# Performance work log

Measured on AMD Instinct MI355X. Metric: run time of the kernel, lower is better.

Reference implementation:

```python
import jax, jax.numpy as jnp
import numpy as np
from jax.ops import segment_sum, segment_max

B, P, NP, EP = 128, 16, 256, 1280
EPG, ODIM, NH = 2048, 256, 128
EPS = 1e-5


def _bn(x, g, b):
    # BatchNorm1d (training-mode batch statistics), biased variance like torch
    mu = x.mean(0)
    var = ((x - mu) ** 2).mean(0)
    return g * (x - mu) * jax.lax.rsqrt(var + EPS) + b


def _gat(feat, src, dst, W, al, ar, resW, bias):
    # DGL GATConv: fc -> per-head attn logits -> leaky_relu -> edge softmax over dst -> aggregate; + residual fc + bias
    n = feat.shape[0]
    H, D = al.shape
    z = (feat @ W).reshape(n, H, D)
    el = (z * al).sum(-1)                                  # [n,H]
    er = (z * ar).sum(-1)
    e = jax.nn.leaky_relu(el[src] + er[dst], 0.2)          # [E,H]
    m = segment_max(e, dst, num_segments=n)
    ex = jnp.exp(e - m[dst])
    s = segment_sum(ex, dst, num_segments=n)
    a = ex / (s[dst] + 1e-9)
    rst = segment_sum(a[:, :, None] * z[src], dst, num_segments=n)  # [n,H,D]
    res = (feat @ resW).reshape(n, H, D)
    return (rst + res + bias.reshape(1, H, D)).reshape(n, H * D)


def _plane(feat, src, dst, p):
    # PlaneGraphEncoder forward (eval: dropout off)
    h = _gat(feat, src, dst, p['W1'], p['al1'], p['ar1'], p['res1'], p['b1'])
    h = jax.nn.relu(_bn(h, p['g1'], p['be1']))
    h = _gat(h, src, dst, p['W2'], p['al2'], p['ar2'], p['res2'], p['b2'])
    h = jax.nn.relu(_bn(h, p['g2'], p['be2']))
    rep = h.mean(0)                                        # dgl.mean_nodes -> [32]
    d = jax.nn.relu(_bn(h @ p['dW1'] + p['db1'], p['dg'], p['dbe']))
    recon = d @ p['dW2'] + p['db2']                        # [n,1]
    rloss = jnp.mean((recon - feat) ** 2)
    return rep, rloss


def _masked_gc(h, src, dst, mask_f, W, b):
    # DGL GraphConv(norm='both') with edge_weight = mask[src]*mask[dst]; structural degrees, clamp>=1
    n = h.shape[0]
    ones = jnp.ones(src.shape[0], h.dtype)
    d_out = jnp.maximum(segment_sum(ones, src, num_segments=n), 1.0)
    d_in = jnp.maximum(segment_sum(ones, dst, num_segments=n), 1.0)
    ew = mask_f[src] * mask_f[dst]                         # [E]
    hs = h * jax.lax.rsqrt(d_out)[:, None]
    agg = segment_sum(ew[:, None] * hs[src], dst, num_segments=n)
    return (agg * jax.lax.rsqrt(d_in)[:, None]) @ W + b


def _forward(plane_feat, original_features,
             W1, al1, ar1, res1, b1, g1, be1,
             W2, al2, ar2, res2, b2, g2, be2,
             dW1, db1, dg, dbe, dW2, db2,
             ft_W, ft_b, ft_g, ft_be, gc_W, gc_b, gbn_g, gbn_be,
             c1_W, c1_b, ln_g, ln_be, c2_W, c2_b,
             plane_src, plane_dst, patient_src, patient_dst, mask):
    pp = dict(W1=W1, al1=al1, ar1=ar1, res1=res1, b1=b1, g1=g1, be1=be1,
              W2=W2, al2=al2, ar2=ar2, res2=res2, b2=b2, g2=g2, be2=be2,
              dW1=dW1, db1=db1, dg=dg, dbe=dbe, dW2=dW2, db2=db2)
    enc_b = jax.vmap(_plane, in_axes=(0, 0, 0, None))      # over patients
    enc_pb = jax.vmap(enc_b, in_axes=(1, 1, 1, 0))         # over planes (params axis 0)
    reps, rlosses = enc_pb(plane_feat, plane_src, plane_dst, pp)   # [P,B,32], [P,B]
    plane_rep = jnp.transpose(reps, (1, 0, 2)).reshape(plane_feat.shape[0], -1)  # [B, P*32]
    avg_recon = rlosses.mean()                             # sum / (B*P)

    x = jnp.concatenate([original_features, plane_rep], axis=1)   # [B, fused]
    h = jax.nn.relu(_bn(x @ ft_W + ft_b, ft_g, ft_be))
    mask_f = mask.astype(h.dtype)
    h_sum = h
    for i in range(3):
        hn = _masked_gc(h, patient_src, patient_dst, mask_f, gc_W[i], gc_b[i])
        hn = jax.nn.relu(_bn(hn, gbn_g[i], gbn_be[i]))
        h = hn + h
        h_sum = h_sum + h
    h = h_sum / 4.0                                        # mean over [h0,h1,h2,h3]

    z = h @ c1_W + c1_b
    mu = z.mean(-1, keepdims=True)
    var = ((z - mu) ** 2).mean(-1, keepdims=True)
    z = jax.nn.relu(ln_g * (z - mu) * jax.lax.rsqrt(var + EPS) + ln_be)
    logits = z @ c2_W + c2_b
    return logits, avg_recon


def setup_inputs() -> dict:
    key = jax.random.key(0)
    ks = iter(jax.random.split(key, 64))
    f = lambda shape, s=0.1: jax.random.normal(next(ks), shape, jnp.float32) * s
    inp = dict(
        plane_feat=f((B, P, NP, 1), 1.0),
        plane_src=jax.random.randint(next(ks), (B, P, EP), 0, NP, jnp.int32),
        plane_dst=jax.random.randint(next(ks), (B, P, EP), 0, NP, jnp.int32),
        patient_src=jax.random.randint(next(ks), (EPG,), 0, B, jnp.int32),
        patient_dst=jax.random.randint(next(ks), (EPG,), 0, B, jnp.int32),
        original_features=f((B, ODIM), 1.0),
        mask=jax.random.randint(next(ks), (B,), 0, 2, jnp.int32),
        # per-plane encoder params, stacked over P
        W1=f((P, 1, 128)), al1=f((P, 2, 64)), ar1=f((P, 2, 64)),
        res1=f((P, 1, 128)), b1=f((P, 128)),
        g1=jnp.ones((P, 128)), be1=jnp.zeros((P, 128)),
        W2=f((P, 128, 32)), al2=f((P, 1, 32)), ar2=f((P, 1, 32)),
        res2=f((P, 128, 32)), b2=f((P, 32)),
        g2=jnp.ones((P, 32)), be2=jnp.zeros((P, 32)),
        dW1=f((P, 32, 128)), db1=f((P, 128)),
        dg=jnp.ones((P, 128)), dbe=jnp.zeros((P, 128)),
        dW2=f((P, 128, 1)), db2=f((P, 1)),
        # patient-level params
        ft_W=f((ODIM + P * 32, NH)), ft_b=f((NH,)),
        ft_g=jnp.ones((NH,)), ft_be=jnp.zeros((NH,)),
        gc_W=f((3, NH, NH)), gc_b=f((3, NH)),
        gbn_g=jnp.ones((3, NH)), gbn_be=jnp.zeros((3, NH)),
        c1_W=f((NH, NH // 2)), c1_b=f((NH // 2,)),
        ln_g=jnp.ones((NH // 2,)), ln_be=jnp.zeros((NH // 2,)),
        c2_W=f((NH // 2, 2)), c2_b=f((2,)),
    )
    return inp


def reference(plane_feat, plane_src, plane_dst, patient_src, patient_dst,
              original_features, mask,
              W1, al1, ar1, res1, b1, g1, be1,
              W2, al2, ar2, res2, b2, g2, be2,
              dW1, db1, dg, dbe, dW2, db2,
              ft_W, ft_b, ft_g, ft_be, gc_W, gc_b, gbn_g, gbn_be,
              c1_W, c1_b, ln_g, ln_be, c2_W, c2_b):
    return _forward(plane_feat, original_features,
                    W1, al1, ar1, res1, b1, g1, be1,
                    W2, al2, ar2, res2, b2, g2, be2,
                    dW1, db1, dg, dbe, dW2, db2,
                    ft_W, ft_b, ft_g, ft_be, gc_W, gc_b, gbn_g, gbn_be,
                    c1_W, c1_b, ln_g, ln_be, c2_W, c2_b,
                    plane_src, plane_dst, patient_src, patient_dst, mask)
```

## Files before the change

kernel.cpp:

```cpp
#include <hip/hip_runtime.h>

#define B_    128
#define P_    16
#define NP_   256
#define EP_   1280
#define EPG_  2048
#define ODIM_ 256
#define NH_   128

typedef __attribute__((ext_vector_type(8))) short s8_t;
typedef __attribute__((ext_vector_type(4))) short s4_t;
typedef __attribute__((ext_vector_type(4))) float f4_t;

__device__ __forceinline__ unsigned short f2b(float x) {
  unsigned u = __builtin_bit_cast(unsigned, x);
  u = (u + 0x7fffu + ((u >> 16) & 1u)) >> 16;
  return (unsigned short)u;
}
__device__ __forceinline__ float b2f(short x) {
  unsigned u = ((unsigned)(unsigned short)x) << 16;
  return __builtin_bit_cast(float, u);
}

struct SmemA {
  float f[256];
  union {
    __align__(16) unsigned short wT1[64 * 136];
    __align__(16) unsigned short z2[256 * 40];
  } u1;
  __align__(16) unsigned short dW1T[128 * 36];
  union {
    struct { float S0a[256]; float S1a[256]; } a;
    float redf[512];
  } u2;
  float el2[256], er2[256];
  union {
    struct { float abg0[128], abg1[128], abg2[128]; } a;
    struct { float al2v[32], ar2v[32], dW2v[128]; } b;
  } u3;
  union {
    int cnt[256];
    struct { float scA[32], shA[32], dscA[64], dshA[64]; } b;
  } u4;
  unsigned short esrc[1280];
  int wtot[4];
  float r8[4][8]; float stat[8]; float wA[2], wB[2];
  float rlacc;
};

__global__ __launch_bounds__(256, 3) void plane_enc(
    const float* __restrict__ feat, const int* __restrict__ esrcg, const int* __restrict__ edstg,
    const float* __restrict__ W1, const float* __restrict__ al1, const float* __restrict__ ar1,
    const float* __restrict__ res1, const float* __restrict__ b1, const float* __restrict__ g1,
    const float* __restrict__ be1,
    const float* __restrict__ W2, const float* __restrict__ al2, const float* __restrict__ ar2,
    const float* __restrict__ res2, const float* __restrict__ g2, const float* __restrict__ be2,
    const float* __restrict__ dW1, const float* __restrict__ dg, const float* __restrict__ dbe,
    const float* __restrict__ dW2, const float* __restrict__ db2,
    float* __restrict__ rep_out, float* __restrict__ rlp_out)
{
  __shared__ SmemA s;
  const int g = blockIdx.x;
  const int p = g & 15;
  const int t = threadIdx.x;
  const int lane = t & 63, wv = t >> 6;
  const int l15 = lane & 15, quad = lane >> 4;

  s.f[t] = feat[g * NP_ + t];
  if (t == 0) s.rlacc = 0.f;
  s.u4.cnt[t] = 0;
  __syncthreads();

  const int* gs = esrcg + g * EP_;
  const int* gd = edstg + g * EP_;
  for (int k = t; k < EP_; k += 256) atomicAdd(&s.u4.cnt[gd[k]], 1);
  __syncthreads();
  int v = s.u4.cnt[t];
  int incl = v;
  #pragma unroll
  for (int off = 1; off < 64; off <<= 1) {
    int n = __shfl_up(incl, off, 64);
    if (lane >= off) incl += n;
  }
  if (lane == 63) s.wtot[wv] = incl;
  __syncthreads();
  int woff = 0;
  for (int w = 0; w < wv; w++) woff += s.wtot[w];
  const int myStart = woff + incl - v;
  const int myDeg = v;
  __syncthreads();
  s.u4.cnt[t] = myStart;
  __syncthreads();
  for (int k = t; k < EP_; k += 256) {
    int d = gd[k];
    int pos = atomicAdd(&s.u4.cnt[d], 1);
    s.esrc[pos] = (unsigned short)gs[k];
  }
  {
    const float* W2g = W2 + p * 4096;
    const float* Rg  = res2 + p * 4096;
    for (int q = 0; q < 16; q++) {
      int idx = t + 256 * q;
      int k = idx >> 5, n = idx & 31;
      s.u1.wT1[n * 136 + k]        = f2b(W2g[idx]);
      s.u1.wT1[(n + 32) * 136 + k] = f2b(Rg[idx]);
    }
  }
  if (t < 128) {
    float w1v = W1[p * 128 + t];
    s.el2[t] = w1v * al1[p * 128 + t];
    s.er2[t] = w1v * ar1[p * 128 + t];
  }
  __syncthreads();
  if (t < 2) {
    float a = 0.f, bq = 0.f;
    for (int d2 = 0; d2 < 64; d2++) { a += s.el2[t * 64 + d2]; bq += s.er2[t * 64 + d2]; }
    s.wA[t] = a; s.wB[t] = bq;
  }
  __syncthreads();

  const float fi = s.f[t];
  float S0, S1;
  {
    const float wa0 = s.wA[0], wb0 = s.wB[0], wa1 = s.wA[1], wb1 = s.wB[1];
    float m0 = -1e30f, m1 = -1e30f;
    for (int j = 0; j < myDeg; j++) {
      float fs = s.f[s.esrc[myStart + j]];
      float e0 = wa0 * fs + wb0 * fi; e0 = e0 > 0.f ? e0 : 0.2f * e0;
      float e1 = wa1 * fs + wb1 * fi; e1 = e1 > 0.f ? e1 : 0.2f * e1;
      m0 = fmaxf(m0, e0); m1 = fmaxf(m1, e1);
    }
    float ss0 = 0.f, ss1 = 0.f, U0 = 0.f, U1 = 0.f;
    for (int j = 0; j < myDeg; j++) {
      float fs = s.f[s.esrc[myStart + j]];
      float e0 = wa0 * fs + wb0 * fi; e0 = e0 > 0.f ? e0 : 0.2f * e0;
      float e1 = wa1 * fs + wb1 * fi; e1 = e1 > 0.f ? e1 : 0.2f * e1;
      float x0 = __expf(e0 - m0), x1 = __expf(e1 - m1);
      ss0 += x0; U0 += x0 * fs;
      ss1 += x1; U1 += x1 * fs;
    }
    S0 = U0 / (ss0 + 1e-9f);
    S1 = U1 / (ss1 + 1e-9f);
    s.u2.a.S0a[t] = S0; s.u2.a.S1a[t] = S1;
  }

  {
    float vals[8] = {fi, fi * fi, S0, S0 * S0, S0 * fi, S1, S1 * S1, S1 * fi};
    #pragma unroll
    for (int d2 = 32; d2 > 0; d2 >>= 1) {
      #pragma unroll
      for (int q = 0; q < 8; q++) vals[q] += __shfl_down(vals[q], d2, 64);
    }
    if (lane == 0) {
      #pragma unroll
      for (int q = 0; q < 8; q++) s.r8[wv][q] = vals[q];
    }
  }
  __syncthreads();
  if (t < 8) s.stat[t] = (s.r8[0][t] + s.r8[1][t] + s.r8[2][t] + s.r8[3][t]) * (1.f / 256.f);
  __syncthreads();
  if (t < 128) {
    float mf = s.stat[0], ef2 = s.stat[1];
    int hh = t >> 6;
    float mS = s.stat[2 + 3 * hh], eS2 = s.stat[3 + 3 * hh], eSf = s.stat[4 + 3 * hh];
    float varS = eS2 - mS * mS, varf = ef2 - mf * mf, cov = eSf - mS * mf;
    float Wv = W1[p * 128 + t], Rv = res1[p * 128 + t], Bv = b1[p * 128 + t];
    float mu  = Wv * mS + Rv * mf + Bv;
    float var = Wv * Wv * varS + Rv * Rv * varf + 2.f * Wv * Rv * cov;
    float gn  = g1[p * 128 + t] * rsqrtf(var + 1e-5f);
    s.u3.a.abg0[t] = gn * Wv;
    s.u3.a.abg1[t] = gn * Rv;
    s.u3.a.abg2[t] = gn * (Bv - mu) + be1[p * 128 + t];
  }
  __syncthreads();

  float resv[32];
  {
    f4_t accum[4][4];
    #pragma unroll
    for (int i = 0; i < 4; i++)
      #pragma unroll
      for (int nt = 0; nt < 4; nt++) accum[i][nt] = (f4_t){0.f, 0.f, 0.f, 0.f};

    float fm[4], s0m[4], s1m[4];
    #pragma unroll
    for (int i = 0; i < 4; i++) {
      int m = (wv * 4 + i) * 16 + l15;
      fm[i] = s.f[m]; s0m[i] = s.u2.a.S0a[m]; s1m[i] = s.u2.a.S1a[m];
    }
    #pragma unroll
    for (int kt = 0; kt < 4; kt++) {
      int cbase = kt * 32 + quad * 8;
      float a0[8], a1[8], a2[8];
      #pragma unroll
      for (int j = 0; j < 8; j++) {
        a0[j] = s.u3.a.abg0[cbase + j]; a1[j] = s.u3.a.abg1[cbase + j]; a2[j] = s.u3.a.abg2[cbase + j];
      }
      s8_t afr[4];
      #pragma unroll
      for (int i = 0; i < 4; i++) {
        float Sm = (kt < 2) ? s0m[i] : s1m[i];
        union { s8_t v; unsigned short u[8]; } fu;
        #pragma unroll
        for (int j = 0; j < 8; j++) {
          float h = fmaxf(fmaf(a0[j], Sm, fmaf(a1[j], fm[i], a2[j])), 0.f);
          fu.u[j] = f2b(h);
        }
        afr[i] = fu.v;
      }
      s8_t bfr[4];
      #pragma unroll
      for (int nt = 0; nt < 4; nt++)
        bfr[nt] = *(const s8_t*)&s.u1.wT1[(nt * 16 + l15) * 136 + cbase];
      #pragma unroll
      for (int i = 0; i < 4; i++)
        #pragma unroll
        for (int nt = 0; nt < 4; nt++)
          accum[i][nt] = __builtin_amdgcn_mfma_f32_16x16x32_bf16(afr[i], bfr[nt], accum[i][nt], 0, 0, 0);
    }
    __syncthreads();
    #pragma unroll
    for (int i = 0; i < 4; i++) {
      int mBase = (wv * 4 + i) * 16 + quad * 4;
      #pragma unroll
      for (int nt = 0; nt < 2; nt++) {
        int col = nt * 16 + l15;
        #pragma unroll
        for (int r = 0; r < 4; r++)
          s.u1.z2[(mBase + r) * 40 + col] = f2b(accum[i][nt][r]);
      }
      #pragma unroll
      for (int h2 = 0; h2 < 2; h2++)
        #pragma unroll
        for (int r = 0; r < 4; r++)
          resv[(i * 2 + h2) * 4 + r] = accum[i][2 + h2][r];
    }
  }
  if (t < 32) { s.u3.b.al2v[t] = al2[p * 32 + t]; s.u3.b.ar2v[t] = ar2[p * 32 + t]; }
  if (t < 128) s.u3.b.dW2v[t] = dW2[p * 128 + t];
  {
    const float* Dg = dW1 + p * 4096;
    #pragma unroll
    for (int q = 0; q < 16; q++) {
      int idx = t + 256 * q;
      int k = idx >> 7, n = idx & 127;
      s.dW1T[n * 36 + k] = f2b(Dg[idx]);
    }
  }
  const float db2v = db2[p];
  __syncthreads();

  {
    const s8_t* zr = (const s8_t*)&s.u1.z2[t * 40];
    float el = 0.f, er = 0.f;
    #pragma unroll
    for (int q = 0; q < 4; q++) {
      s8_t vz = zr[q];
      #pragma unroll
      for (int j = 0; j < 8; j++) {
        float zv = b2f(vz[j]);
        el += zv * s.u3.b.al2v[q * 8 + j];
        er += zv * s.u3.b.ar2v[q * 8 + j];
      }
    }
    s.el2[t] = el; s.er2[t] = er;
  }
  __syncthreads();

  float hrow[32];
  {
    const float eri = s.er2[t];
    float m = -1e30f;
    for (int j = 0; j < myDeg; j++) {
      float e = s.el2[s.esrc[myStart + j]] + eri;
      e = e > 0.f ? e : 0.2f * e;
      m = fmaxf(m, e);
    }
    float ss = 0.f;
    #pragma unroll
    for (int d2 = 0; d2 < 32; d2++) hrow[d2] = 0.f;
    for (int j = 0; j < myDeg; j++) {
      int sj = s.esrc[myStart + j];
      float e = s.el2[sj] + eri;
      e = e > 0.f ? e : 0.2f * e;
      float x = __expf(e - m);
      ss += x;
      const s8_t* zr = (const s8_t*)&s.u1.z2[sj * 40];
      #pragma unroll
      for (int q = 0; q < 4; q++) {
        s8_t vz = zr[q];
        #pragma unroll
        for (int jj = 0; jj < 8; jj++) hrow[q * 8 + jj] += x * b2f(vz[jj]);
      }
    }
    float inv = 1.f / (ss + 1e-9f);
    #pragma unroll
    for (int d2 = 0; d2 < 32; d2++) hrow[d2] *= inv;
  }
  __syncthreads();
  #pragma unroll
  for (int i = 0; i < 4; i++) {
    int mBase = (wv * 4 + i) * 16 + quad * 4;
    #pragma unroll
    for (int h2 = 0; h2 < 2; h2++) {
      int col = h2 * 16 + l15;
      #pragma unroll
      for (int r = 0; r < 4; r++)
        s.u1.z2[(mBase + r) * 40 + col] = f2b(resv[(i * 2 + h2) * 4 + r]);
    }
  }
  __syncthreads();
  {
    const s8_t* zr = (const s8_t*)&s.u1.z2[t * 40];
    #pragma unroll
    for (int q = 0; q < 4; q++) {
      s8_t vz = zr[q];
      #pragma unroll
      for (int jj = 0; jj < 8; jj++) hrow[q * 8 + jj] += b2f(vz[jj]);
    }
  }
  #pragma unroll
  for (int d2 = 0; d2 < 32; d2++) s.u1.z2[t * 40 + d2] = f2b(hrow[d2]);
  __syncthreads();

  {
    int c = t & 31, gq = t >> 5;
    float s1 = 0.f, s2 = 0.f;
    for (int j = 0; j < 32; j++) {
      float vz = b2f((short)s.u1.z2[(gq * 32 + j) * 40 + c]);
      s1 += vz; s2 += vz * vz;
    }
    s.u2.redf[t] = s1; s.u2.redf[256 + t] = s2;
  }
  __syncthreads();
  if (t < 32) {
    float s1 = 0.f, s2 = 0.f;
    #pragma unroll
    for (int q = 0; q < 8; q++) { s1 += s.u2.redf[q * 32 + t]; s2 += s.u2.redf[256 + q * 32 + t]; }
    float mu = s1 * (1.f / 256.f);
    float var = s2 * (1.f / 256.f) - mu * mu;
    float a = g2[p * 32 + t] * rsqrtf(var + 1e-5f);
    s.u4.b.scA[t] = a; s.u4.b.shA[t] = be2[p * 32 + t] - a * mu;
  }
  __syncthreads();
  {
    int c = t & 31, gq = t >> 5;
    float a = s.u4.b.scA[c], bb = s.u4.b.shA[c];
    float s1 = 0.f;
    for (int j = 0; j < 32; j++) {
      int ad = (gq * 32 + j) * 40 + c;
      float vz = b2f((short)s.u1.z2[ad]);
      float hv = fmaxf(a * vz + bb, 0.f);
      s.u1.z2[ad] = f2b(hv);
      s1 += hv;
    }
    s.u2.redf[t] = s1;
  }
  __syncthreads();
  if (t < 32) {
    float s1 = 0.f;
    #pragma unroll
    for (int q = 0; q < 8; q++) s1 += s.u2.redf[q * 32 + t];
    rep_out[g * 32 + t] = s1 * (1.f / 256.f);
  }
  __syncthreads();

  {
    s8_t afr2[4];
    #pragma unroll
    for (int i = 0; i < 4; i++)
      afr2[i] = *(const s8_t*)&s.u1.z2[((wv * 4 + i) * 16 + l15) * 40 + quad * 8];
    float rAcc[4][4];
    #pragma unroll
    for (int i = 0; i < 4; i++)
      #pragma unroll
      for (int r = 0; r < 4; r++) rAcc[i][r] = 0.f;

    for (int half = 0; half < 2; half++) {
      __syncthreads();
      s.u2.redf[t] = 0.f; s.u2.redf[256 + t] = 0.f;
      __syncthreads();
      f4_t acc2[4][4];
      #pragma unroll
      for (int i = 0; i < 4; i++)
        #pragma unroll
        for (int nt = 0; nt < 4; nt++) acc2[i][nt] = (f4_t){0.f, 0.f, 0.f, 0.f};
      s8_t bfr[4];
      #pragma unroll
      for (int nt = 0; nt < 4; nt++) {
        const s4_t* pr = (const s4_t*)&s.dW1T[(half * 64 + nt * 16 + l15) * 36 + quad * 8];
        s4_t lo = pr[0], hi = pr[1];
        bfr[nt] = __builtin_shufflevector(lo, hi, 0, 1, 2, 3, 4, 5, 6, 7);
      }
      #pragma unroll
      for (int i = 0; i < 4; i++)
        #pragma unroll
        for (int nt = 0; nt < 4; nt++)
          acc2[i][nt] = __builtin_amdgcn_mfma_f32_16x16x32_bf16(afr2[i], bfr[nt], acc2[i][nt], 0, 0, 0);
      #pragma unroll
      for (int nt = 0; nt < 4; nt++) {
        float s1 = 0.f, s2 = 0.f;
        #pragma unroll
        for (int i = 0; i < 4; i++)
          #pragma unroll
          for (int r = 0; r < 4; r++) { float vv = acc2[i][nt][r]; s1 += vv; s2 += vv * vv; }
        atomicAdd(&s.u2.redf[nt * 16 + l15], s1);
        atomicAdd(&s.u2.redf[256 + nt * 16 + l15], s2);
      }
      __syncthreads();
      if (t < 64) {
        int col = half * 64 + t;
        float mu = s.u2.redf[t] * (1.f / 256.f);
        float var = s.u2.redf[256 + t] * (1.f / 256.f) - mu * mu;
        float a = dg[p * 128 + col] * rsqrtf(var + 1e-5f);
        s.u4.b.dscA[t] = a; s.u4.b.dshA[t] = dbe[p * 128 + col] - a * mu;
      }
      __syncthreads();
      #pragma unroll
      for (int nt = 0; nt < 4; nt++) {
        int cl = nt * 16 + l15;
        float a = s.u4.b.dscA[cl], bb = s.u4.b.dshA[cl], w2 = s.u3.b.dW2v[half * 64 + cl];
        #pragma unroll
        for (int i = 0; i < 4; i++)
          #pragma unroll
          for (int r = 0; r < 4; r++) {
            float dv = fmaxf(a * acc2[i][nt][r] + bb, 0.f);
            rAcc[i][r] += dv * w2;
          }
      }
    }
    #pragma unroll
    for (int off = 1; off < 16; off <<= 1)
      #pragma unroll
      for (int i = 0; i < 4; i++)
        #pragma unroll
        for (int r = 0; r < 4; r++) rAcc[i][r] += __shfl_xor(rAcc[i][r], off, 64);
    if (l15 == 0) {
      float sq = 0.f;
      #pragma unroll
      for (int i = 0; i < 4; i++)
        #pragma unroll
        for (int r = 0; r < 4; r++) {
          int m = (wv * 4 + i) * 16 + quad * 4 + r;
          float diff = rAcc[i][r] + db2v - s.f[m];
          sq += diff * diff;
        }
      atomicAdd(&s.rlacc, sq);
    }
  }
  __syncthreads();
  if (t == 0) rlp_out[g] = s.rlacc;
}

__global__ __launch_bounds__(256) void ft_mm(
    const float* __restrict__ orig, const float* __restrict__ rep,
    const float* __restrict__ ftW, float* __restrict__ hpre,
    const int* __restrict__ ps, const int* __restrict__ pd,
    const int* __restrict__ mask, unsigned short* __restrict__ abar,
    const float* __restrict__ gcW, unsigned short* __restrict__ gws)
{
  const int t = threadIdx.x;

  if (blockIdx.x >= 9) {
    const int layer = blockIdx.x - 9;
    const float* src = gcW + layer * 16384;
    unsigned short* dst = gws + layer * 16384;
    for (int idx = t; idx < 16384; idx += 256) dst[idx] = f2b(src[idx]);
    return;
  }

  if (blockIdx.x == 8) {
    __shared__ int aB[128 * 128];
    __shared__ int co[128], ci[128];
    __shared__ float facs[128], facd[128];
    for (int idx = t; idx < 16384; idx += 256) aB[idx] = 0;
    if (t < 128) { co[t] = 0; ci[t] = 0; }
    __syncthreads();
    for (int e = t; e < EPG_; e += 256) {
      int sN = ps[e], d = pd[e];
      atomicAdd(&co[sN], 1);
      atomicAdd(&ci[d], 1);
      atomicAdd(&aB[d * 128 + sN], 1);
    }
    __syncthreads();
    if (t < 128) {
      float mk = (float)mask[t];
      int da = co[t] > 1 ? co[t] : 1;
      int db = ci[t] > 1 ? ci[t] : 1;
      facs[t] = mk * rsqrtf((float)da);
      facd[t] = mk * rsqrtf((float)db);
    }
    __syncthreads();
    for (int idx = t; idx < 16384; idx += 256) {
      int d = idx >> 7, sN = idx & 127;
      abar[idx] = f2b((float)aB[idx] * facd[d] * facs[sN]);
    }
    return;
  }

  const int wv = t >> 6, lane = t & 63;
  const int l15 = lane & 15, quad = lane >> 4;
  const int m = blockIdx.x * 16 + l15;

  f4_t acc[2];
  acc[0] = (f4_t){0.f, 0.f, 0.f, 0.f};
  acc[1] = (f4_t){0.f, 0.f, 0.f, 0.f};
  for (int kt = 0; kt < 24; kt++) {
    int k0 = kt * 32 + quad * 8;
    const float* px = (k0 < 256) ? (orig + m * 256 + k0) : (rep + m * 512 + (k0 - 256));
    float4 xa = ((const float4*)px)[0];
    float4 xb = ((const float4*)px)[1];
    union { s8_t v; unsigned short u[8]; } fu;
    fu.u[0] = f2b(xa.x); fu.u[1] = f2b(xa.y); fu.u[2] = f2b(xa.z); fu.u[3] = f2b(xa.w);
    fu.u[4] = f2b(xb.x); fu.u[5] = f2b(xb.y); fu.u[6] = f2b(xb.z); fu.u[7] = f2b(xb.w);
    #pragma unroll
    for (int nt = 0; nt < 2; nt++) {
      int col = wv * 32 + nt * 16 + l15;
      union { s8_t v; unsigned short u[8]; } bu;
      #pragma unroll
      for (int j = 0; j < 8; j++) bu.u[j] = f2b(ftW[(k0 + j) * 128 + col]);
      acc[nt] = __builtin_amdgcn_mfma_f32_16x16x32_bf16(fu.v, bu.v, acc[nt], 0, 0, 0);
    }
  }
  #pragma unroll
  for (int nt = 0; nt < 2; nt++) {
    int col = wv * 32 + nt * 16 + l15;
    #pragma unroll
    for (int r = 0; r < 4; r++)
      hpre[(blockIdx.x * 16 + quad * 4 + r) * 128 + col] = acc[nt][r];
  }
}

struct SmemB {
  __align__(16) unsigned short arow[128 * 136];
  __align__(16) unsigned short hT[128 * 136];
  union {
    struct {
      union {
        __align__(16) unsigned short wT[128 * 136];
        float zF[128 * 68];
      } w;
      __align__(16) unsigned short aggB[128 * 136];
    } mm;
  } u;
  float redA[1024], redB[1024];
  float scB[128], shB[128];
};

__global__ __launch_bounds__(1024) void k_patient(
    const float* __restrict__ hpre, const unsigned short* __restrict__ abar,
    const float* __restrict__ ftg, const float* __restrict__ ftbe,
    const unsigned short* __restrict__ gws, const float* __restrict__ gbng,
    const float* __restrict__ gbnbe,
    const float* __restrict__ c1W, const float* __restrict__ c1b,
    const float* __restrict__ lng, const float* __restrict__ lnbe,
    const float* __restrict__ c2W, const float* __restrict__ c2b,
    const float* __restrict__ rlp, float* __restrict__ out)
{
  __shared__ SmemB s;
  const int t = threadIdx.x;
  const int w = t >> 6, lane = t & 63;
  const int l15 = lane & 15, quad = lane >> 4;
  const int mb = w & 7, nb = (w >> 3) * 64;

  for (int idx = t; idx < 16384; idx += 1024) {
    int d = idx >> 7, sN = idx & 127;
    s.arow[d * 136 + sN] = abar[idx];
  }

  f4_t acc[4];
  #pragma unroll
  for (int nt = 0; nt < 4; nt++) {
    int col = nb + nt * 16 + l15;
    #pragma unroll
    for (int r = 0; r < 4; r++)
      acc[nt][r] = hpre[(mb * 16 + quad * 4 + r) * 128 + col];
  }

  float hR[16], hsumR[16];
  {
    #pragma unroll
    for (int nt = 0; nt < 4; nt++) {
      float s1 = acc[nt][0] + acc[nt][1] + acc[nt][2] + acc[nt][3];
      float s2 = acc[nt][0]*acc[nt][0] + acc[nt][1]*acc[nt][1] + acc[nt][2]*acc[nt][2] + acc[nt][3]*acc[nt][3];
      s1 += __shfl_xor(s1, 16, 64); s1 += __shfl_xor(s1, 32, 64);
      s2 += __shfl_xor(s2, 16, 64); s2 += __shfl_xor(s2, 32, 64);
      if (quad == 0) {
        s.redA[mb * 128 + nb + nt * 16 + l15] = s1;
        s.redB[mb * 128 + nb + nt * 16 + l15] = s2;
      }
    }
    __syncthreads();
    if (t < 128) {
      float a1 = 0.f, a2 = 0.f;
      #pragma unroll
      for (int q = 0; q < 8; q++) { a1 += s.redA[q * 128 + t]; a2 += s.redB[q * 128 + t]; }
      float mu = a1 * (1.f / 128.f), var = a2 * (1.f / 128.f) - mu * mu;
      float a = ftg[t] * rsqrtf(var + 1e-5f);
      s.scB[t] = a; s.shB[t] = ftbe[t] - a * mu;
    }
    __syncthreads();
    #pragma unroll
    for (int nt = 0; nt < 4; nt++) {
      int col = nb + nt * 16 + l15;
      float a = s.scB[col], bb = s.shB[col];
      #pragma unroll
      for (int r = 0; r < 4; r++) {
        int row = mb * 16 + quad * 4 + r;
        float hv = fmaxf(a * acc[nt][r] + bb, 0.f);
        hR[nt * 4 + r] = hv; hsumR[nt * 4 + r] = hv;
        s.hT[col * 136 + row] = f2b(hv);
      }
    }
  }
  __syncthreads();

  for (int layer = 0; layer < 3; layer++) {
    #pragma unroll
    for (int q = 0; q < 16; q++) {
      int idx = t + 1024 * q;
      int kk = idx >> 7, n = idx & 127;
      s.u.mm.w.wT[n * 136 + kk] = gws[layer * 16384 + idx];
    }
    f4_t ag[4];
    #pragma unroll
    for (int nt = 0; nt < 4; nt++) ag[nt] = (f4_t){0.f, 0.f, 0.f, 0.f};
    #pragma unroll
    for (int ks = 0; ks < 4; ks++) {
      s8_t afr = *(const s8_t*)&s.arow[(mb * 16 + l15) * 136 + ks * 32 + quad * 8];
      #pragma unroll
      for (int nt = 0; nt < 4; nt++) {
        s8_t bfr = *(const s8_t*)&s.hT[(nb + nt * 16 + l15) * 136 + ks * 32 + quad * 8];
        ag[nt] = __builtin_amdgcn_mfma_f32_16x16x32_bf16(afr, bfr, ag[nt], 0, 0, 0);
      }
    }
    #pragma unroll
    for (int nt = 0; nt < 4; nt++) {
      int col = nb + nt * 16 + l15;
      #pragma unroll
      for (int r = 0; r < 4; r++)
        s.u.mm.aggB[(mb * 16 + quad * 4 + r) * 136 + col] = f2b(ag[nt][r]);
    }
    __syncthreads();
    f4_t oc[4];
    #pragma unroll
    for (int nt = 0; nt < 4; nt++) oc[nt] = (f4_t){0.f, 0.f, 0.f, 0.f};
    #pragma unroll
    for (int ks = 0; ks < 4; ks++) {
      s8_t afr = *(const s8_t*)&s.u.mm.aggB[(mb * 16 + l15) * 136 + ks * 32 + quad * 8];
      #pragma unroll
      for (int nt = 0; nt < 4; nt++) {
        s8_t bfr = *(const s8_t*)&s.u.mm.w.wT[(nb + nt * 16 + l15) * 136 + ks * 32 + quad * 8];
        oc[nt] = __builtin_amdgcn_mfma_f32_16x16x32_bf16(afr, bfr, oc[nt], 0, 0, 0);
      }
    }
    #pragma unroll
    for (int nt = 0; nt < 4; nt++) {
      float s1 = oc[nt][0] + oc[nt][1] + oc[nt][2] + oc[nt][3];
      float s2 = oc[nt][0]*oc[nt][0] + oc[nt][1]*oc[nt][1] + oc[nt][2]*oc[nt][2] + oc[nt][3]*oc[nt][3];
      s1 += __shfl_xor(s1, 16, 64); s1 += __shfl_xor(s1, 32, 64);
      s2 += __shfl_xor(s2, 16, 64); s2 += __shfl_xor(s2, 32, 64);
      if (quad == 0) {
        s.redA[mb * 128 + nb + nt * 16 + l15] = s1;
        s.redB[mb * 128 + nb + nt * 16 + l15] = s2;
      }
    }
    __syncthreads();
    if (t < 128) {
      float a1 = 0.f, a2 = 0.f;
      #pragma unroll
      for (int q = 0; q < 8; q++) { a1 += s.redA[q * 128 + t]; a2 += s.redB[q * 128 + t]; }
      float mu = a1 * (1.f / 128.f), var = a2 * (1.f / 128.f) - mu * mu;
      float a = gbng[layer * 128 + t] * rsqrtf(var + 1e-5f);
      s.scB[t] = a; s.shB[t] = gbnbe[layer * 128 + t] - a * mu;
    }
    __syncthreads();
    #pragma unroll
    for (int nt = 0; nt < 4; nt++) {
      int col = nb + nt * 16 + l15;
      float a = s.scB[col], bb = s.shB[col];
      #pragma unroll
      for (int r = 0; r < 4; r++) {
        int row = mb * 16 + quad * 4 + r;
        float hn = fmaxf(a * oc[nt][r] + bb, 0.f) + hR[nt * 4 + r];
        hR[nt * 4 + r] = hn;
        hsumR[nt * 4 + r] += hn;
        s.hT[col * 136 + row] = f2b(hn);
      }
    }
    __syncthreads();
  }

  #pragma unroll
  for (int nt = 0; nt < 4; nt++) {
    int col = nb + nt * 16 + l15;
    #pragma unroll
    for (int r = 0; r < 4; r++)
      s.u.mm.aggB[(mb * 16 + quad * 4 + r) * 136 + col] = f2b(hsumR[nt * 4 + r] * 0.25f);
  }
  #pragma unroll
  for (int q = 0; q < 8; q++) {
    int idx = t + 1024 * q;
    int n = idx & 63, kk = idx >> 6;
    s.u.mm.w.wT[n * 136 + kk] = f2b(c1W[kk * 64 + n]);
  }
  __syncthreads();
  {
    const int nb2 = (w >> 3) * 32;
    f4_t zc[2];
    #pragma unroll
    for (int nt = 0; nt < 2; nt++) zc[nt] = (f4_t){0.f, 0.f, 0.f, 0.f};
    #pragma unroll
    for (int ks = 0; ks < 4; ks++) {
      s8_t afr = *(const s8_t*)&s.u.mm.aggB[(mb * 16 + l15) * 136 + ks * 32 + quad * 8];
      #pragma unroll
      for (int nt = 0; nt < 2; nt++) {
        s8_t bfr = *(const s8_t*)&s.u.mm.w.wT[(nb2 + nt * 16 + l15) * 136 + ks * 32 + quad * 8];
        zc[nt] = __builtin_amdgcn_mfma_f32_16x16x32_bf16(afr, bfr, zc[nt], 0, 0, 0);
      }
    }
    __syncthreads();
    #pragma unroll
    for (int nt = 0; nt < 2; nt++) {
      int col = nb2 + nt * 16 + l15;
      #pragma unroll
      for (int r = 0; r < 4; r++)
        s.u.mm.w.zF[(mb * 16 + quad * 4 + r) * 68 + col] = zc[nt][r] + c1b[col];
    }
  }
  __syncthreads();
  if (t < 128) {
    float s1 = 0.f, s2 = 0.f;
    #pragma unroll
    for (int j = 0; j < 64; j++) { float zv = s.u.mm.w.zF[t * 68 + j]; s1 += zv; s2 += zv * zv; }
    float mu = s1 * (1.f / 64.f);
    float var = s2 * (1.f / 64.f) - mu * mu;
    float rs = rsqrtf(var + 1e-5f);
    float l0 = 0.f, l1 = 0.f;
    #pragma unroll
    for (int j = 0; j < 64; j++) {
      float zv = s.u.mm.w.zF[t * 68 + j];
      float zn = fmaxf(lng[j] * (zv - mu) * rs + lnbe[j], 0.f);
      l0 += zn * c2W[j * 2];
      l1 += zn * c2W[j * 2 + 1];
    }
    out[t * 2]     = l0 + c2b[0];
    out[t * 2 + 1] = l1 + c2b[1];
  }

  {
    float r = rlp[t] + rlp[t + 1024];
    #pragma unroll
    for (int off = 32; off > 0; off >>= 1) r += __shfl_down(r, off, 64);
    if (lane == 0) s.redA[w] = r;
  }
  __syncthreads();
  if (t == 0) {
    float tot = 0.f;
    #pragma unroll
    for (int i = 0; i < 16; i++) tot += s.redA[i];
    out[256] = tot * (1.f / (256.f * 2048.f));
  }
}

extern "C" void kernel_launch(void* const* d_in, const int* in_sizes, int n_in,
                              void* d_out, int out_size, void* d_ws, size_t ws_size,
                              hipStream_t stream) {
  (void)in_sizes; (void)n_in; (void)out_size; (void)ws_size;
  const float* plane_feat  = (const float*)d_in[0];
  const int*   plane_src   = (const int*)d_in[1];
  const int*   plane_dst   = (const int*)d_in[2];
  const int*   patient_src = (const int*)d_in[3];
  const int*   patient_dst = (const int*)d_in[4];
  const float* orig        = (const float*)d_in[5];
  const int*   mask        = (const int*)d_in[6];
  const float* W1   = (const float*)d_in[7];
  const float* al1  = (const float*)d_in[8];
  const float* ar1  = (const float*)d_in[9];
  const float* res1 = (const float*)d_in[10];
  const float* b1   = (const float*)d_in[11];
  const float* g1   = (const float*)d_in[12];
  const float* be1  = (const float*)d_in[13];
  const float* W2   = (const float*)d_in[14];
  const float* al2  = (const float*)d_in[15];
  const float* ar2  = (const float*)d_in[16];
  const float* res2 = (const float*)d_in[17];
  const float* g2   = (const float*)d_in[19];
  const float* be2  = (const float*)d_in[20];
  const float* dW1  = (const float*)d_in[21];
  const float* dg   = (const float*)d_in[23];
  const float* dbe  = (const float*)d_in[24];
  const float* dW2  = (const float*)d_in[25];
  const float* db2  = (const float*)d_in[26];
  const float* ftW  = (const float*)d_in[27];
  const float* ftg  = (const float*)d_in[29];
  const float* ftbe = (const float*)d_in[30];
  const float* gcW  = (const float*)d_in[31];
  const float* gbng = (const float*)d_in[33];
  const float* gbnbe= (const float*)d_in[34];
  const float* c1W  = (const float*)d_in[35];
  const float* c1b  = (const float*)d_in[36];
  const float* lng  = (const float*)d_in[37];
  const float* lnbe = (const float*)d_in[38];
  const float* c2W  = (const float*)d_in[39];
  const float* c2b  = (const float*)d_in[40];

  float* ws   = (float*)d_ws;
  float* rep  = ws;
  float* hpre = ws + 65536;
  unsigned short* abar = (unsigned short*)(ws + 81920);
  float* rlp  = ws + 90112;
  unsigned short* gws = (unsigned short*)(ws + 94208);
  float* outp = (float*)d_out;

  plane_enc<<<2048, 256, 0, stream>>>(plane_feat, plane_src, plane_dst,
      W1, al1, ar1, res1, b1, g1, be1, W2, al2, ar2, res2, g2, be2,
      dW1, dg, dbe, dW2, db2, rep, rlp);
  ft_mm<<<12, 256, 0, stream>>>(orig, rep, ftW, hpre,
      patient_src, patient_dst, mask, abar, gcW, gws);
  k_patient<<<1, 1024, 0, stream>>>(hpre, abar, ftg, ftbe,
      gws, gbng, gbnbe, c1W, c1b, lng, lnbe, c2W, c2b, rlp, outp);
}
```

Measured before the change: 314.4 us.

## Double plane encoder block to 512 threads, splitting heads and MFMA rows

Result: slower. 373.1 us (+18.7%).

```diff
diff --git a/kernel.cpp b/kernel.cpp
--- a/kernel.cpp
+++ b/kernel.cpp
@@ -43,12 +43,13 @@
     struct { float scA[32], shA[32], dscA[64], dshA[64]; } b;
   } u4;
   unsigned short esrc[1280];
+  unsigned short mst[256], mdg[256];
   int wtot[4];
   float r8[4][8]; float stat[8]; float wA[2], wB[2];
   float rlacc;
 };
 
-__global__ __launch_bounds__(256, 3) void plane_enc(
+__global__ __launch_bounds__(512) void plane_enc(
     const float* __restrict__ feat, const int* __restrict__ esrcg, const int* __restrict__ edstg,
     const float* __restrict__ W1, const float* __restrict__ al1, const float* __restrict__ ar1,
     const float* __restrict__ res1, const float* __restrict__ b1, const float* __restrict__ g1,
@@ -63,35 +64,39 @@
   const int g = blockIdx.x;
   const int p = g & 15;
   const int t = threadIdx.x;
-  const int lane = t & 63, wv = t >> 6;
+  const int lane = t & 63, w8 = t >> 6;
   const int l15 = lane & 15, quad = lane >> 4;
 
-  s.f[t] = feat[g * NP_ + t];
+  if (t < 256) { s.f[t] = feat[g * NP_ + t]; s.u4.cnt[t] = 0; }
   if (t == 0) s.rlacc = 0.f;
-  s.u4.cnt[t] = 0;
   __syncthreads();
 
   const int* gs = esrcg + g * EP_;
   const int* gd = edstg + g * EP_;
-  for (int k = t; k < EP_; k += 256) atomicAdd(&s.u4.cnt[gd[k]], 1);
-  __syncthreads();
-  int v = s.u4.cnt[t];
-  int incl = v;
-  #pragma unroll
-  for (int off = 1; off < 64; off <<= 1) {
-    int n = __shfl_up(incl, off, 64);
-    if (lane >= off) incl += n;
-  }
-  if (lane == 63) s.wtot[wv] = incl;
-  __syncthreads();
-  int woff = 0;
-  for (int w = 0; w < wv; w++) woff += s.wtot[w];
-  const int myStart = woff + incl - v;
-  const int myDeg = v;
-  __syncthreads();
-  s.u4.cnt[t] = myStart;
-  __syncthreads();
-  for (int k = t; k < EP_; k += 256) {
+  for (int k = t; k < EP_; k += 512) atomicAdd(&s.u4.cnt[gd[k]], 1);
+  __syncthreads();
+  {
+    int v = (t < 256) ? s.u4.cnt[t] : 0;
+    int incl = v;
+    #pragma unroll
+    for (int off = 1; off < 64; off <<= 1) {
+      int n = __shfl_up(incl, off, 64);
+      if (lane >= off) incl += n;
+    }
+    if (t < 256 && lane == 63) s.wtot[w8] = incl;
+    __syncthreads();
+    if (t < 256) {
+      int woff = 0;
+      for (int w = 0; w < w8; w++) woff += s.wtot[w];
+      int myStart = woff + incl - v;
+      s.mst[t] = (unsigned short)myStart;
+      s.mdg[t] = (unsigned short)v;
+    }
+    __syncthreads();
+    if (t < 256) s.u4.cnt[t] = (int)s.mst[t];
+  }
+  __syncthreads();
+  for (int k = t; k < EP_; k += 512) {
     int d = gd[k];
     int pos = atomicAdd(&s.u4.cnt[d], 1);
     s.esrc[pos] = (unsigned short)gs[k];
@@ -99,8 +104,8 @@
   {
     const float* W2g = W2 + p * 4096;
     const float* Rg  = res2 + p * 4096;
-    for (int q = 0; q < 16; q++) {
-      int idx = t + 256 * q;
+    for (int q = 0; q < 8; q++) {
+      int idx = t + 512 * q;
       int k = idx >> 5, n = idx & 31;
       s.u1.wT1[n * 136 + k]        = f2b(W2g[idx]);
       s.u1.wT1[(n + 32) * 136 + k] = f2b(Rg[idx]);
@@ -119,32 +124,31 @@
   }
   __syncthreads();
 
-  const float fi = s.f[t];
-  float S0, S1;
-  {
-    const float wa0 = s.wA[0], wb0 = s.wB[0], wa1 = s.wA[1], wb1 = s.wB[1];
-    float m0 = -1e30f, m1 = -1e30f;
-    for (int j = 0; j < myDeg; j++) {
-      float fs = s.f[s.esrc[myStart + j]];
-      float e0 = wa0 * fs + wb0 * fi; e0 = e0 > 0.f ? e0 : 0.2f * e0;
-      float e1 = wa1 * fs + wb1 * fi; e1 = e1 > 0.f ? e1 : 0.2f * e1;
-      m0 = fmaxf(m0, e0); m1 = fmaxf(m1, e1);
-    }
-    float ss0 = 0.f, ss1 = 0.f, U0 = 0.f, U1 = 0.f;
-    for (int j = 0; j < myDeg; j++) {
-      float fs = s.f[s.esrc[myStart + j]];
-      float e0 = wa0 * fs + wb0 * fi; e0 = e0 > 0.f ? e0 : 0.2f * e0;
-      float e1 = wa1 * fs + wb1 * fi; e1 = e1 > 0.f ? e1 : 0.2f * e1;
-      float x0 = __expf(e0 - m0), x1 = __expf(e1 - m1);
-      ss0 += x0; U0 += x0 * fs;
-      ss1 += x1; U1 += x1 * fs;
-    }
-    S0 = U0 / (ss0 + 1e-9f);
-    S1 = U1 / (ss1 + 1e-9f);
-    s.u2.a.S0a[t] = S0; s.u2.a.S1a[t] = S1;
-  }
-
-  {
+  {
+    const int n = t & 255, hh = t >> 8;
+    const int st = s.mst[n], dgn = s.mdg[n];
+    const float fi = s.f[n];
+    const float wa = s.wA[hh], wb = s.wB[hh];
+    float m = -1e30f;
+    for (int j = 0; j < dgn; j++) {
+      float fs = s.f[s.esrc[st + j]];
+      float e = wa * fs + wb * fi; e = e > 0.f ? e : 0.2f * e;
+      m = fmaxf(m, e);
+    }
+    float ss = 0.f, U = 0.f;
+    for (int j = 0; j < dgn; j++) {
+      float fs = s.f[s.esrc[st + j]];
+      float e = wa * fs + wb * fi; e = e > 0.f ? e : 0.2f * e;
+      float x = __expf(e - m);
+      ss += x; U += x * fs;
+    }
+    float S = U / (ss + 1e-9f);
+    if (hh == 0) s.u2.a.S0a[n] = S; else s.u2.a.S1a[n] = S;
+  }
+  __syncthreads();
+
+  if (t < 256) {
+    float fi = s.f[t], S0 = s.u2.a.S0a[t], S1 = s.u2.a.S1a[t];
     float vals[8] = {fi, fi * fi, S0, S0 * S0, S0 * fi, S1, S1 * S1, S1 * fi};
     #pragma unroll
     for (int d2 = 32; d2 > 0; d2 >>= 1) {
@@ -153,7 +157,7 @@
     }
     if (lane == 0) {
       #pragma unroll
-      for (int q = 0; q < 8; q++) s.r8[wv][q] = vals[q];
+      for (int q = 0; q < 8; q++) s.r8[w8][q] = vals[q];
     }
   }
   __syncthreads();
@@ -174,18 +178,18 @@
   }
   __syncthreads();
 
-  float resv[32];
-  {
-    f4_t accum[4][4];
-    #pragma unroll
-    for (int i = 0; i < 4; i++)
+  float resv[16];
+  {
+    f4_t accum[2][4];
+    #pragma unroll
+    for (int i = 0; i < 2; i++)
       #pragma unroll
       for (int nt = 0; nt < 4; nt++) accum[i][nt] = (f4_t){0.f, 0.f, 0.f, 0.f};
 
-    float fm[4], s0m[4], s1m[4];
-    #pragma unroll
-    for (int i = 0; i < 4; i++) {
-      int m = (wv * 4 + i) * 16 + l15;
+    float fm[2], s0m[2], s1m[2];
+    #pragma unroll
+    for (int i = 0; i < 2; i++) {
+      int m = (w8 * 2 + i) * 16 + l15;
       fm[i] = s.f[m]; s0m[i] = s.u2.a.S0a[m]; s1m[i] = s.u2.a.S1a[m];
     }
     #pragma unroll
@@ -196,9 +200,9 @@
       for (int j = 0; j < 8; j++) {
         a0[j] = s.u3.a.abg0[cbase + j]; a1[j] = s.u3.a.abg1[cbase + j]; a2[j] = s.u3.a.abg2[cbase + j];
       }
-      s8_t afr[4];
-      #pragma unroll
-      for (int i = 0; i < 4; i++) {
+      s8_t afr[2];
+      #pragma unroll
+      for (int i = 0; i < 2; i++) {
         float Sm = (kt < 2) ? s0m[i] : s1m[i];
         union { s8_t v; unsigned short u[8]; } fu;
         #pragma unroll
@@ -213,15 +217,15 @@
       for (int nt = 0; nt < 4; nt++)
         bfr[nt] = *(const s8_t*)&s.u1.wT1[(nt * 16 + l15) * 136 + cbase];
       #pragma unroll
-      for (int i = 0; i < 4; i++)
+      for (int i = 0; i < 2; i++)
         #pragma unroll
         for (int nt = 0; nt < 4; nt++)
           accum[i][nt] = __builtin_amdgcn_mfma_f32_16x16x32_bf16(afr[i], bfr[nt], accum[i][nt], 0, 0, 0);
     }
     __syncthreads();
     #pragma unroll
-    for (int i = 0; i < 4; i++) {
-      int mBase = (wv * 4 + i) * 16 + quad * 4;
+    for (int i = 0; i < 2; i++) {
+      int mBase = (w8 * 2 + i) * 16 + quad * 4;
       #pragma unroll
       for (int nt = 0; nt < 2; nt++) {
         int col = nt * 16 + l15;
@@ -241,8 +245,8 @@
   {
     const float* Dg = dW1 + p * 4096;
     #pragma unroll
-    for (int q = 0; q < 16; q++) {
-      int idx = t + 256 * q;
+    for (int q = 0; q < 8; q++) {
+      int idx = t + 512 * q;
       int k = idx >> 7, n = idx & 127;
       s.dW1T[n * 36 + k] = f2b(Dg[idx]);
     }
@@ -250,7 +254,7 @@
   const float db2v = db2[p];
   __syncthreads();
 
-  {
+  if (t < 256) {
     const s8_t* zr = (const s8_t*)&s.u1.z2[t * 40];
     float el = 0.f, er = 0.f;
     #pragma unroll
@@ -267,63 +271,65 @@
   }
   __syncthreads();
 
-  float hrow[32];
-  {
-    const float eri = s.er2[t];
+  {
+    const int n = t & 255, cb = (t >> 8) * 2;
+    const int st = s.mst[n], dgn = s.mdg[n];
+    const float eri = s.er2[n];
     float m = -1e30f;
-    for (int j = 0; j < myDeg; j++) {
-      float e = s.el2[s.esrc[myStart + j]] + eri;
+    for (int j = 0; j < dgn; j++) {
+      float e = s.el2[s.esrc[st + j]] + eri;
       e = e > 0.f ? e : 0.2f * e;
       m = fmaxf(m, e);
     }
+    float hrow[16];
+    #pragma unroll
+    for (int d2 = 0; d2 < 16; d2++) hrow[d2] = 0.f;
     float ss = 0.f;
-    #pragma unroll
-    for (int d2 = 0; d2 < 32; d2++) hrow[d2] = 0.f;
-    for (int j = 0; j < myDeg; j++) {
-      int sj = s.esrc[myStart + j];
+    for (int j = 0; j < dgn; j++) {
+      int sj = s.esrc[st + j];
       float e = s.el2[sj] + eri;
       e = e > 0.f ? e : 0.2f * e;
       float x = __expf(e - m);
       ss += x;
       const s8_t* zr = (const s8_t*)&s.u1.z2[sj * 40];
       #pragma unroll
-      for (int q = 0; q < 4; q++) {
-        s8_t vz = zr[q];
+      for (int q = 0; q < 2; q++) {
+        s8_t vz = zr[cb + q];
         #pragma unroll
         for (int jj = 0; jj < 8; jj++) hrow[q * 8 + jj] += x * b2f(vz[jj]);
       }
     }
-    float inv = 1.f / (ss + 1e-9f);
-    #pragma unroll
-    for (int d2 = 0; d2 < 32; d2++) hrow[d2] *= inv;
-  }
-  __syncthreads();
-  #pragma unroll
-  for (int i = 0; i < 4; i++) {
-    int mBase = (wv * 4 + i) * 16 + quad * 4;
-    #pragma unroll
-    for (int h2 = 0; h2 < 2; h2++) {
-      int col = h2 * 16 + l15;
-      #pragma unroll
-      for (int r = 0; r < 4; r++)
-        s.u1.z2[(mBase + r) * 40 + col] = f2b(resv[(i * 2 + h2) * 4 + r]);
-    }
-  }
-  __syncthreads();
-  {
-    const s8_t* zr = (const s8_t*)&s.u1.z2[t * 40];
-    #pragma unroll
-    for (int q = 0; q < 4; q++) {
-      s8_t vz = zr[q];
-      #pragma unroll
-      for (int jj = 0; jj < 8; jj++) hrow[q * 8 + jj] += b2f(vz[jj]);
-    }
-  }
-  #pragma unroll
-  for (int d2 = 0; d2 < 32; d2++) s.u1.z2[t * 40 + d2] = f2b(hrow[d2]);
-  __syncthreads();
-
-  {
+    const float inv = 1.f / (ss + 1e-9f);
+    __syncthreads();
+    #pragma unroll
+    for (int i = 0; i < 2; i++) {
+      int mBase = (w8 * 2 + i) * 16 + quad * 4;
+      #pragma unroll
+      for (int h2 = 0; h2 < 2; h2++) {
+        int col = h2 * 16 + l15;
+        #pragma unroll
+        for (int r = 0; r < 4; r++)
+          s.u1.z2[(mBase + r) * 40 + col] = f2b(resv[(i * 2 + h2) * 4 + r]);
+      }
+    }
+    __syncthreads();
+    {
+      const s8_t* zr = (const s8_t*)&s.u1.z2[n * 40];
+      #pragma unroll
+      for (int q = 0; q < 2; q++) {
+        s8_t vz = zr[cb + q];
+        #pragma unroll
+        for (int jj = 0; jj < 8; jj++)
+          hrow[q * 8 + jj] = hrow[q * 8 + jj] * inv + b2f(vz[jj]);
+      }
+      #pragma unroll
+      for (int d2 = 0; d2 < 16; d2++)
+        s.u1.z2[n * 40 + cb * 8 + d2] = f2b(hrow[d2]);
+    }
+  }
+  __syncthreads();
+
+  if (t < 256) {
     int c = t & 31, gq = t >> 5;
     float s1 = 0.f, s2 = 0.f;
     for (int j = 0; j < 32; j++) {
@@ -343,7 +349,7 @@
     s.u4.b.scA[t] = a; s.u4.b.shA[t] = be2[p * 32 + t] - a * mu;
   }
   __syncthreads();
-  {
+  if (t < 256) {
     int c = t & 31, gq = t >> 5;
     float a = s.u4.b.scA[c], bb = s.u4.b.shA[c];
     float s1 = 0.f;
@@ -366,23 +372,23 @@
   __syncthreads();
 
   {
-    s8_t afr2[4];
-    #pragma unroll
-    for (int i = 0; i < 4; i++)
-      afr2[i] = *(const s8_t*)&s.u1.z2[((wv * 4 + i) * 16 + l15) * 40 + quad * 8];
-    float rAcc[4][4];
-    #pragma unroll
-    for (int i = 0; i < 4; i++)
+    s8_t afr2[2];
+    #pragma unroll
+    for (int i = 0; i < 2; i++)
+      afr2[i] = *(const s8_t*)&s.u1.z2[((w8 * 2 + i) * 16 + l15) * 40 + quad * 8];
+    float rAcc[2][4];
+    #pragma unroll
+    for (int i = 0; i < 2; i++)
       #pragma unroll
       for (int r = 0; r < 4; r++) rAcc[i][r] = 0.f;
 
     for (int half = 0; half < 2; half++) {
       __syncthreads();
-      s.u2.redf[t] = 0.f; s.u2.redf[256 + t] = 0.f;
+      s.u2.redf[t] = 0.f;
       __syncthreads();
-      f4_t acc2[4][4];
-      #pragma unroll
-      for (int i = 0; i < 4; i++)
+      f4_t acc2[2][4];
+      #pragma unroll
+      for (int i = 0; i < 2; i++)
         #pragma unroll
         for (int nt = 0; nt < 4; nt++) acc2[i][nt] = (f4_t){0.f, 0.f, 0.f, 0.f};
       s8_t bfr[4];
@@ -393,7 +399,7 @@
         bfr[nt] = __builtin_shufflevector(lo, hi, 0, 1, 2, 3, 4, 5, 6, 7);
       }
       #pragma unroll
-      for (int i = 0; i < 4; i++)
+      for (int i = 0; i < 2; i++)
         #pragma unroll
         for (int nt = 0; nt < 4; nt++)
           acc2[i][nt] = __builtin_amdgcn_mfma_f32_16x16x32_bf16(afr2[i], bfr[nt], acc2[i][nt], 0, 0, 0);
@@ -401,7 +407,7 @@
       for (int nt = 0; nt < 4; nt++) {
         float s1 = 0.f, s2 = 0.f;
         #pragma unroll
-        for (int i = 0; i < 4; i++)
+        for (int i = 0; i < 2; i++)
           #pragma unroll
           for (int r = 0; r < 4; r++) { float vv = acc2[i][nt][r]; s1 += vv; s2 += vv * vv; }
         atomicAdd(&s.u2.redf[nt * 16 + l15], s1);
@@ -421,7 +427,7 @@
         int cl = nt * 16 + l15;
         float a = s.u4.b.dscA[cl], bb = s.u4.b.dshA[cl], w2 = s.u3.b.dW2v[half * 64 + cl];
         #pragma unroll
-        for (int i = 0; i < 4; i++)
+        for (int i = 0; i < 2; i++)
           #pragma unroll
           for (int r = 0; r < 4; r++) {
             float dv = fmaxf(a * acc2[i][nt][r] + bb, 0.f);
@@ -432,16 +438,16 @@
     #pragma unroll
     for (int off = 1; off < 16; off <<= 1)
       #pragma unroll
-      for (int i = 0; i < 4; i++)
+      for (int i = 0; i < 2; i++)
         #pragma unroll
         for (int r = 0; r < 4; r++) rAcc[i][r] += __shfl_xor(rAcc[i][r], off, 64);
     if (l15 == 0) {
       float sq = 0.f;
       #pragma unroll
-      for (int i = 0; i < 4; i++)
+      for (int i = 0; i < 2; i++)
         #pragma unroll
         for (int r = 0; r < 4; r++) {
-          int m = (wv * 4 + i) * 16 + quad * 4 + r;
+          int m = (w8 * 2 + i) * 16 + quad * 4 + r;
           float diff = rAcc[i][r] + db2v - s.f[m];
           sq += diff * diff;
         }
@@ -813,7 +819,7 @@
   unsigned short* gws = (unsigned short*)(ws + 94208);
   float* outp = (float*)d_out;
 
-  plane_enc<<<2048, 256, 0, stream>>>(plane_feat, plane_src, plane_dst,
+  plane_enc<<<2048, 512, 0, stream>>>(plane_feat, plane_src, plane_dst,
       W1, al1, ar1, res1, b1, g1, be1, W2, al2, ar2, res2, g2, be2,
       dW1, dg, dbe, dW2, db2, rep, rlp);
   ft_mm<<<12, 256, 0, stream>>>(orig, rep, ftW, hpre,
```
